# Kernel optimization log

Measured on AMD Instinct MI355X. Metric: run time of the kernel, lower is better.

The kernel has to match this reference:

```python
import jax, jax.numpy as jnp
import numpy as np

B, S, DM, H, NL, DFF = 2, 1024, 1024, 16, 4, 4096
HD = DM // H
MAX_LEN = 1024
NUM_REL = 2 * MAX_LEN - 1
EPS = 1e-5


def setup_inputs() -> dict:
    key = jax.random.key(0)
    ks = jax.random.split(key, 10)
    w = lambda k, shp: jax.random.normal(k, shp, jnp.float32) * 0.02
    return {
        "x": jax.random.normal(ks[0], (B, S, DM), jnp.float32),
        "Wq": w(ks[1], (NL, DM, DM)), "bq": jnp.zeros((NL, DM), jnp.float32),
        "Wk": w(ks[2], (NL, DM, DM)), "bk": jnp.zeros((NL, DM), jnp.float32),
        "Wv": w(ks[3], (NL, DM, DM)), "bv": jnp.zeros((NL, DM), jnp.float32),
        "Wo": w(ks[4], (NL, DM, DM)), "bo": jnp.zeros((NL, DM), jnp.float32),
        "rel": w(ks[5], (NL, NUM_REL, HD)),
        "W1": w(ks[6], (NL, DFF, DM)), "b1": jnp.zeros((NL, DFF), jnp.float32),
        "W2": w(ks[7], (NL, DM, DFF)), "b2": jnp.zeros((NL, DM), jnp.float32),
        "g1": jnp.ones((NL, DM), jnp.float32), "beta1": jnp.zeros((NL, DM), jnp.float32),
        "g2": jnp.ones((NL, DM), jnp.float32), "beta2": jnp.zeros((NL, DM), jnp.float32),
    }


def _layer_norm(y, g, b):
    m = y.mean(-1, keepdims=True)
    v = ((y - m) ** 2).mean(-1, keepdims=True)
    return (y - m) / jnp.sqrt(v + EPS) * g + b


def _forward(x, Wq, bq, Wk, bk, Wv, bv, Wo, bo, rel, W1, b1, W2, b2, g1, beta1, g2, beta2):
    scale = np.sqrt(HD).astype(np.float32)
    # relative position index matrix: idx[j,k] = k - j + S - 1  (values in [0, 2S-2])
    idx = (jnp.arange(S)[None, :] - jnp.arange(S)[:, None]) + S - 1

    def layer(xc, p):
        (Wq_, bq_, Wk_, bk_, Wv_, bv_, Wo_, bo_, rel_,
         W1_, b1_, W2_, b2_, g1_, be1_, g2_, be2_) = p

        def proj(W, b):
            return (xc @ W.T + b).reshape(B, S, H, HD).transpose(0, 2, 1, 3)  # [B,H,S,HD]

        Q, K, V = proj(Wq_, bq_), proj(Wk_, bk_), proj(Wv_, bv_)
        scores = jnp.einsum('bhid,bhjd->bhij', Q, K) / scale
        # einsum('bhid,jkd->bhijk', Q, rel[idx]).mean(-1) == Q @ mean_k(rel[idx])^T
        Ebar = rel_[idx].mean(axis=1)  # [S, HD]
        scores = scores + jnp.einsum('bhid,jd->bhij', Q, Ebar)
        attn = jax.nn.softmax(scores, axis=-1)
        out = jnp.einsum('bhij,bhjd->bhid', attn, V)
        out = out.transpose(0, 2, 1, 3).reshape(B, S, DM) @ Wo_.T + bo_
        xc = _layer_norm(xc + out, g1_, be1_)
        h = jax.nn.gelu(xc @ W1_.T + b1_, approximate=False)
        ff = h @ W2_.T + b2_
        xc = _layer_norm(xc + ff, g2_, be2_)
        return xc, None

    stacked = (Wq, bq, Wk, bk, Wv, bv, Wo, bo, rel, W1, b1, W2, b2, g1, beta1, g2, beta2)
    out, _ = jax.lax.scan(layer, x, stacked)
    return out


def reference(x, Wq, bq, Wk, bk, Wv, bv, Wo, bo, rel, W1, b1, W2, b2, g1, beta1, g2, beta2):
    return _forward(x, Wq, bq, Wk, bk, Wv, bv, Wo, bo, rel, W1, b1, W2, b2, g1, beta1, g2, beta2)
```

## Files before the change

### kernel.cpp

```cpp
#include <hip/hip_runtime.h>
#include <math.h>

typedef __attribute__((ext_vector_type(4))) float f32x4;
typedef __attribute__((ext_vector_type(8))) short s16x8;
typedef __attribute__((ext_vector_type(8))) unsigned short u16x8;
typedef __attribute__((ext_vector_type(4))) unsigned short u16x4;

#define DI __device__ __forceinline__

DI unsigned short f2bf(float f) {
  unsigned int u = __builtin_bit_cast(unsigned int, f);
  u = u + 0x7fffu + ((u >> 16) & 1u);
  return (unsigned short)(u >> 16);
}

DI void gload16(const unsigned short* g, unsigned short* l) {
  __builtin_amdgcn_global_load_lds(
      (const __attribute__((address_space(1))) void*)g,
      (__attribute__((address_space(3))) void*)l, 16, 0, 0);
}

__global__ __launch_bounds__(256) void cvtw_k(const float* __restrict__ src,
    unsigned short* __restrict__ dst, int chunk, int dstStride, int total4)
{
  for (int i = blockIdx.x * 256 + threadIdx.x; i < total4; i += gridDim.x * 256) {
    int idx = i * 4;
    int blk = idx / chunk, off = idx - blk * chunk;
    f32x4 v = *reinterpret_cast<const f32x4*>(src + idx);
    u16x4 o = { f2bf(v[0]), f2bf(v[1]), f2bf(v[2]), f2bf(v[3]) };
    *reinterpret_cast<u16x4*>(dst + (size_t)blk * dstStride + off) = o;
  }
}

__global__ __launch_bounds__(256) void xinit_k(const float* __restrict__ x,
    float* __restrict__ xf, unsigned short* __restrict__ xb, int n4)
{
  for (int i = blockIdx.x * 256 + threadIdx.x; i < n4; i += gridDim.x * 256) {
    f32x4 v = *reinterpret_cast<const f32x4*>(x + (size_t)i * 4);
    *reinterpret_cast<f32x4*>(xf + (size_t)i * 4) = v;
    u16x4 o = { f2bf(v[0]), f2bf(v[1]), f2bf(v[2]), f2bf(v[3]) };
    *reinterpret_cast<u16x4*>(xb + (size_t)i * 4) = o;
  }
}

__global__ __launch_bounds__(64) void ebch_k(const float* __restrict__ rel,
    float* __restrict__ cs)
{
  int c = blockIdx.x, L = blockIdx.y, d = threadIdx.x;
  const float* p = rel + ((size_t)L * 2047 + c * 64) * 64 + d;
  int n = (c == 31) ? 63 : 64;
  float s = 0.f;
  for (int k = 0; k < n; ++k) s += p[(size_t)k * 64];
  cs[(L * 32 + c) * 64 + d] = s;
}

__global__ __launch_bounds__(64) void ebar_k(const float* __restrict__ rel,
    const float* __restrict__ cs, float* __restrict__ ebar4)
{
  int j = blockIdx.x, L = blockIdx.y, d = threadIdx.x;
  int s = 1023 - j, e = s + 1024;
  int c0 = (s + 63) >> 6, c1 = e >> 6;
  const float* rl = rel + (size_t)L * 2047 * 64;
  const float* cl = cs + L * 32 * 64;
  float acc = 0.f;
  for (int c = c0; c < c1; ++c) acc += cl[c * 64 + d];
  for (int t = s; t < c0 * 64; ++t) acc += rl[(size_t)t * 64 + d];
  for (int t = c1 * 64; t < e; ++t) acc += rl[(size_t)t * 64 + d];
  ebar4[((size_t)L * 1024 + j) * 64 + d] = acc * (1.f / 1024.f);
}

template<int BF32, int BN>
__global__ __launch_bounds__(256) void gemm_k(
    const unsigned short* __restrict__ A, const void* __restrict__ Bp,
    int K, int N, int mode, int kLen,
    const float* __restrict__ bias0, const float* __restrict__ bias1,
    const float* __restrict__ bias2, const float* __restrict__ ebar,
    unsigned short* __restrict__ qb, unsigned short* __restrict__ kb,
    unsigned short* __restrict__ vtb, float* __restrict__ yf,
    unsigned short* __restrict__ hb)
{
  constexpr int NI = BN / 32;
  constexpr int WC = BN / 2;
  constexpr int SMSZ = (128 + BN) * 64 > 128 * (BN + 8) ? (128 + BN) * 64 : 128 * (BN + 8);
  __shared__ __align__(16) unsigned short SM[SMSZ];
  auto As = reinterpret_cast<unsigned short(*)[64]>(SM);
  auto Bs = reinterpret_cast<unsigned short(*)[64]>(SM + 128 * 64);
  const int tid = threadIdx.x, l = tid & 63, w = tid >> 6;
  const int wr = w >> 1, wc = w & 1, lr = l & 15, lg = l >> 4;
  const int m0 = blockIdx.y * 128, n0 = blockIdx.x * BN;
  f32x4 acc[4][NI];
#pragma unroll
  for (int i = 0; i < 4; ++i)
#pragma unroll
    for (int j = 0; j < NI; ++j) acc[i][j] = f32x4{0.f, 0.f, 0.f, 0.f};

  const int kBeg = blockIdx.z * kLen, kEnd = kBeg + kLen;
  const unsigned short* gaBase = A + (size_t)(m0 + (l >> 3)) * K + (l & 7) * 8;

  for (int k0 = kBeg; k0 < kEnd; k0 += 64) {
    __syncthreads();
#pragma unroll
    for (int it = 0; it < 4; ++it) {
      int r0 = (w * 4 + it) * 8;
      gload16(gaBase + (size_t)r0 * K + k0, &As[r0][0]);
    }
    if (BF32 == 0) {
      const unsigned short* Bb = (const unsigned short*)Bp;
      const unsigned short* gb = Bb + (size_t)(n0 + (l >> 3)) * K + k0 + (l & 7) * 8;
#pragma unroll
      for (int it = 0; it < BN / 32; ++it) {
        int r0 = (w * (BN / 32) + it) * 8;
        gload16(gb + (size_t)r0 * K, &Bs[r0][0]);
      }
    } else {
      const float* Bf = (const float*)Bp;
#pragma unroll
      for (int it = 0; it < BN / 16; ++it) {
        int lin = (it * 256 + tid) * 4, r = lin >> 6, c = lin & 63;
        f32x4 v = *reinterpret_cast<const f32x4*>(Bf + (size_t)(n0 + r) * K + k0 + c);
        u16x4 o = { f2bf(v[0]), f2bf(v[1]), f2bf(v[2]), f2bf(v[3]) };
        *reinterpret_cast<u16x4*>(&Bs[r][c]) = o;
      }
    }
    __syncthreads();
#pragma unroll
    for (int kk = 0; kk < 2; ++kk) {
      s16x8 af[4], bfr[NI];
#pragma unroll
      for (int mi = 0; mi < 4; ++mi)
        af[mi] = *reinterpret_cast<const s16x8*>(&As[wr * 64 + mi * 16 + lr][kk * 32 + lg * 8]);
#pragma unroll
      for (int ni = 0; ni < NI; ++ni)
        bfr[ni] = *reinterpret_cast<const s16x8*>(&Bs[wc * WC + ni * 16 + lr][kk * 32 + lg * 8]);
#pragma unroll
      for (int mi = 0; mi < 4; ++mi)
#pragma unroll
        for (int ni = 0; ni < NI; ++ni)
          acc[mi][ni] = __builtin_amdgcn_mfma_f32_16x16x32_bf16(af[mi], bfr[ni], acc[mi][ni], 0, 0, 0);
    }
  }

  if (mode <= 3) {
    int qtype, nbase;
    const float* bias;
    if (mode == 0) {
      qtype = n0 >> 10; nbase = n0 & 1023;
      bias = qtype == 0 ? bias0 : (qtype == 1 ? bias1 : bias2);
    } else { qtype = mode - 1; nbase = n0; bias = bias0; }
    if (qtype < 2) {
      unsigned short* dst = (qtype == 0) ? qb : kb;
#pragma unroll
      for (int mi = 0; mi < 4; ++mi)
#pragma unroll
        for (int ni = 0; ni < NI; ++ni) {
          int nin = nbase + wc * WC + ni * 16 + lr;
          int hh = nin >> 6, dh = nin & 63;
          float bv = bias[nin];
#pragma unroll
          for (int rr = 0; rr < 4; ++rr) {
            int m = m0 + wr * 64 + mi * 16 + lg * 4 + rr;
            int b = m >> 10, s = m & 1023;
            float v = acc[mi][ni][rr] + bv;
            if (qtype == 1) v = v * 0.125f + ebar[s * 64 + dh];
            dst[(size_t)(b * 16 + hh) * 65536 + (size_t)s * 64 + dh] = f2bf(v);
          }
        }
    } else {
      auto T = reinterpret_cast<unsigned short(*)[BN + 8]>(SM);
      __syncthreads();
#pragma unroll
      for (int mi = 0; mi < 4; ++mi)
#pragma unroll
        for (int ni = 0; ni < NI; ++ni) {
          int nl = wc * WC + ni * 16 + lr;
          float bv = bias[nbase + nl];
#pragma unroll
          for (int rr = 0; rr < 4; ++rr) {
            int ml = wr * 64 + mi * 16 + lg * 4 + rr;
            T[ml][nl] = f2bf(acc[mi][ni][rr] + bv);
          }
        }
      __syncthreads();
      int b = m0 >> 10, j0 = m0 & 1023;
#pragma unroll
      for (int lp = 0; lp < BN / 16; ++lp) {
        int dl = lp * 16 + (tid >> 4), jc = (tid & 15) * 8;
        u16x8 o;
#pragma unroll
        for (int e = 0; e < 8; ++e) o[e] = T[jc + e][dl];
        int nin = nbase + dl, hh = nin >> 6, dh = nin & 63;
        *reinterpret_cast<u16x8*>(vtb + (size_t)(b * 16 + hh) * 65536 + (size_t)dh * 1024 + j0 + jc) = o;
      }
    }
  } else {
    float* yfp = yf + (size_t)blockIdx.z * 2097152;
#pragma unroll
    for (int mi = 0; mi < 4; ++mi)
#pragma unroll
      for (int ni = 0; ni < NI; ++ni) {
        int nn = n0 + wc * WC + ni * 16 + lr;
        float bv = (blockIdx.z == 0) ? bias0[nn] : 0.f;
#pragma unroll
        for (int rr = 0; rr < 4; ++rr) {
          int m = m0 + wr * 64 + mi * 16 + lg * 4 + rr;
          float v = acc[mi][ni][rr] + bv;
          if (mode == 4) yfp[(size_t)m * N + nn] = v;
          else hb[(size_t)m * N + nn] = f2bf(0.5f * v * (1.f + erff(v * 0.70710678118654752f)));
        }
      }
  }
}

__global__ __launch_bounds__(256, 4) void attn_k(const unsigned short* __restrict__ qb,
    const unsigned short* __restrict__ kb, const unsigned short* __restrict__ vtb,
    float* __restrict__ opart, float* __restrict__ lpart)
{
  __shared__ __align__(16) unsigned short Ks[2][64][72];
  __shared__ __align__(16) unsigned short Vs[64][72];
  __shared__ __align__(16) unsigned short Pl[4][16][72];
  const int id = blockIdx.x;
  const int xcd = id & 7, sub = id >> 3;
  const int bh = xcd * 4 + (sub >> 5);
  const int rest = sub & 31;
  const int tq = rest >> 1, half = rest & 1;
  const int tid = threadIdx.x, l = tid & 63, w = tid >> 6;
  const int lr = l & 15, lg = l >> 4;
  const int jt0 = half * 8;

  const unsigned short* Kb = kb + (size_t)bh * 65536;
  const unsigned short* Vb = vtb + (size_t)bh * 65536;

  const unsigned short* Qp = qb + (size_t)bh * 65536 +
      (size_t)(tq * 64 + w * 16 + lr) * 64 + lg * 8;
  s16x8 qf0 = *reinterpret_cast<const s16x8*>(Qp);
  s16x8 qf1 = *reinterpret_cast<const s16x8*>(Qp + 32);

  const int srow = tid >> 2, scol = (tid & 3) * 16;
  const unsigned short* kg = Kb + (size_t)srow * 64 + scol + (size_t)jt0 * 4096;
  const unsigned short* vg = Vb + (size_t)srow * 1024 + scol + (size_t)jt0 * 64;

  u16x8 krg[2][2], vrg[2][2];
  f32x4 oacc[4];
#pragma unroll
  for (int di = 0; di < 4; ++di) oacc[di] = f32x4{0.f, 0.f, 0.f, 0.f};
  float Lp[4] = { 0.f, 0.f, 0.f, 0.f };

  krg[0][0] = *reinterpret_cast<const u16x8*>(kg);
  krg[0][1] = *reinterpret_cast<const u16x8*>(kg + 8);
  vrg[0][0] = *reinterpret_cast<const u16x8*>(vg);
  vrg[0][1] = *reinterpret_cast<const u16x8*>(vg + 8);
  *reinterpret_cast<u16x8*>(&Ks[0][srow][scol]) = krg[0][0];
  *reinterpret_cast<u16x8*>(&Ks[0][srow][scol + 8]) = krg[0][1];
  krg[1][0] = *reinterpret_cast<const u16x8*>(kg + 4096);
  krg[1][1] = *reinterpret_cast<const u16x8*>(kg + 4096 + 8);
  vrg[1][0] = *reinterpret_cast<const u16x8*>(vg + 64);
  vrg[1][1] = *reinterpret_cast<const u16x8*>(vg + 64 + 8);

#pragma unroll
  for (int it = 0; it < 8; ++it) {
    const int buf = it & 1, nxt = buf ^ 1;
    asm volatile("s_waitcnt lgkmcnt(0)" ::: "memory");
    __builtin_amdgcn_s_barrier();
    __builtin_amdgcn_sched_barrier(0);
    *reinterpret_cast<u16x8*>(&Vs[srow][scol]) = vrg[buf][0];
    *reinterpret_cast<u16x8*>(&Vs[srow][scol + 8]) = vrg[buf][1];
    f32x4 sacc[4];
#pragma unroll
    for (int ni = 0; ni < 4; ++ni) sacc[ni] = f32x4{0.f, 0.f, 0.f, 0.f};
#pragma unroll
    for (int kk = 0; kk < 2; ++kk) {
      s16x8 qq = kk ? qf1 : qf0;
#pragma unroll
      for (int ni = 0; ni < 4; ++ni) {
        s16x8 kf = *reinterpret_cast<const s16x8*>(&Ks[buf][ni * 16 + lr][kk * 32 + lg * 8]);
        sacc[ni] = __builtin_amdgcn_mfma_f32_16x16x32_bf16(qq, kf, sacc[ni], 0, 0, 0);
      }
    }
#pragma unroll
    for (int r = 0; r < 4; ++r) {
#pragma unroll
      for (int ni = 0; ni < 4; ++ni) {
        float p = __expf(fminf(sacc[ni][r], 80.f));
        Lp[r] += p;
        Pl[w][lg * 4 + r][ni * 16 + lr] = f2bf(p);
      }
    }
    asm volatile("s_waitcnt lgkmcnt(0)" ::: "memory");
    __builtin_amdgcn_s_barrier();
    __builtin_amdgcn_sched_barrier(0);
#pragma unroll
    for (int kk = 0; kk < 2; ++kk) {
      s16x8 pa = *reinterpret_cast<const s16x8*>(&Pl[w][lr][kk * 32 + lg * 8]);
#pragma unroll
      for (int di = 0; di < 4; ++di) {
        s16x8 vf = *reinterpret_cast<const s16x8*>(&Vs[di * 16 + lr][kk * 32 + lg * 8]);
        oacc[di] = __builtin_amdgcn_mfma_f32_16x16x32_bf16(pa, vf, oacc[di], 0, 0, 0);
      }
    }
    if (it < 7) {
      *reinterpret_cast<u16x8*>(&Ks[nxt][srow][scol]) = krg[nxt][0];
      *reinterpret_cast<u16x8*>(&Ks[nxt][srow][scol + 8]) = krg[nxt][1];
    }
    if (it < 6) {
      const unsigned short* kp = kg + (size_t)(it + 2) * 4096;
      const unsigned short* vp = vg + (size_t)(it + 2) * 64;
      krg[buf][0] = *reinterpret_cast<const u16x8*>(kp);
      krg[buf][1] = *reinterpret_cast<const u16x8*>(kp + 8);
      vrg[buf][0] = *reinterpret_cast<const u16x8*>(vp);
      vrg[buf][1] = *reinterpret_cast<const u16x8*>(vp + 8);
    }
  }

#pragma unroll
  for (int r = 0; r < 4; ++r) {
#pragma unroll
    for (int xm = 1; xm < 16; xm <<= 1) Lp[r] += __shfl_xor(Lp[r], xm);
  }
  const size_t obase = ((size_t)(half * 32 + bh) * 1024 + tq * 64 + w * 16);
#pragma unroll
  for (int r = 0; r < 4; ++r) {
    int qrow = lg * 4 + r;
#pragma unroll
    for (int di = 0; di < 4; ++di)
      opart[(obase + qrow) * 64 + di * 16 + lr] = oacc[di][r];
    if (lr == 0) lpart[obase + qrow] = Lp[r];
  }
}

__global__ __launch_bounds__(256) void amrg_k(const float* __restrict__ opart,
    const float* __restrict__ lpart, unsigned short* __restrict__ ctx)
{
  int e4 = blockIdx.x * 256 + threadIdx.x;
  int d4 = e4 & 15, q = (e4 >> 4) & 1023, bh = e4 >> 14;
  size_t po = ((size_t)bh * 1024 + q) * 64 + d4 * 4;
  f32x4 o0 = *reinterpret_cast<const f32x4*>(opart + po);
  f32x4 o1 = *reinterpret_cast<const f32x4*>(opart + 2097152 + po);
  float linv = 1.f / (lpart[bh * 1024 + q] + lpart[32768 + bh * 1024 + q]);
  int b = bh >> 4, h = bh & 15;
  u16x4 o;
#pragma unroll
  for (int e = 0; e < 4; ++e) o[e] = f2bf((o0[e] + o1[e]) * linv);
  *reinterpret_cast<u16x4*>(ctx + (size_t)(b * 1024 + q) * 1024 + h * 64 + d4 * 4) = o;
}

__global__ __launch_bounds__(256) void ln_k(const float* __restrict__ xf,
    const float* __restrict__ yf, const float* __restrict__ g,
    const float* __restrict__ be, float* __restrict__ outf,
    unsigned short* __restrict__ outb)
{
  int row = blockIdx.x, tid = threadIdx.x, l = tid & 63, w = tid >> 6;
  size_t base = (size_t)row * 1024 + tid * 4;
  f32x4 v = *reinterpret_cast<const f32x4*>(xf + base);
  f32x4 y0 = *reinterpret_cast<const f32x4*>(yf + base);
  f32x4 y1 = *reinterpret_cast<const f32x4*>(yf + 2097152 + base);
  v = v + y0 + y1;
  float s = v[0] + v[1] + v[2] + v[3];
  float q = v[0] * v[0] + v[1] * v[1] + v[2] * v[2] + v[3] * v[3];
#pragma unroll
  for (int off = 1; off < 64; off <<= 1) { s += __shfl_xor(s, off); q += __shfl_xor(q, off); }
  __shared__ float ss[4], qq[4];
  if (l == 0) { ss[w] = s; qq[w] = q; }
  __syncthreads();
  s = ss[0] + ss[1] + ss[2] + ss[3];
  q = qq[0] + qq[1] + qq[2] + qq[3];
  float m = s * (1.f / 1024.f);
  float var = q * (1.f / 1024.f) - m * m;
  float rs = rsqrtf(var + 1e-5f);
  f32x4 gv = *reinterpret_cast<const f32x4*>(g + tid * 4);
  f32x4 bv = *reinterpret_cast<const f32x4*>(be + tid * 4);
  f32x4 o; u16x4 ob;
#pragma unroll
  for (int e = 0; e < 4; ++e) { o[e] = (v[e] - m) * rs * gv[e] + bv[e]; ob[e] = f2bf(o[e]); }
  *reinterpret_cast<f32x4*>(outf + base) = o;
  *reinterpret_cast<u16x4*>(outb + base) = ob;
}

extern "C" void kernel_launch(void* const* d_in, const int* in_sizes, int n_in,
                              void* d_out, int out_size, void* d_ws, size_t ws_size,
                              hipStream_t stream)
{
  (void)in_sizes; (void)n_in; (void)out_size;
  const float* x   = (const float*)d_in[0];
  const float* Wq  = (const float*)d_in[1];
  const float* bq  = (const float*)d_in[2];
  const float* Wk  = (const float*)d_in[3];
  const float* bk  = (const float*)d_in[4];
  const float* Wv  = (const float*)d_in[5];
  const float* bv  = (const float*)d_in[6];
  const float* Wo  = (const float*)d_in[7];
  const float* bo  = (const float*)d_in[8];
  const float* rel = (const float*)d_in[9];
  const float* W1  = (const float*)d_in[10];
  const float* b1  = (const float*)d_in[11];
  const float* W2  = (const float*)d_in[12];
  const float* b2  = (const float*)d_in[13];
  const float* g1  = (const float*)d_in[14];
  const float* be1 = (const float*)d_in[15];
  const float* g2  = (const float*)d_in[16];
  const float* be2 = (const float*)d_in[17];
  float* out = (float*)d_out;
  char* ws = (char*)d_ws;

  const size_t OFF_XF = 0, OFF_YF = 8388608, OFF_XB = 25165824, OFF_QB = 29360128,
      OFF_KB = 33554432, OFF_VT = 37748736, OFF_CT = 41943040,
      OFF_HB = 46137344 ,
      OFF_LP = 62914560, OFF_EB = 63176704, OFF_CS = 64225280, OFF_W = 64258048;
  const size_t NEED_A = OFF_W + 100663296, NEED_B = OFF_W + 25165824;

  float* xf = (float*)(ws + OFF_XF);
  float* yf = (float*)(ws + OFF_YF);
  unsigned short* xb  = (unsigned short*)(ws + OFF_XB);
  unsigned short* qbp = (unsigned short*)(ws + OFF_QB);
  unsigned short* kbp = (unsigned short*)(ws + OFF_KB);
  unsigned short* vtp = (unsigned short*)(ws + OFF_VT);
  unsigned short* ctx = (unsigned short*)(ws + OFF_CT);
  unsigned short* hb  = (unsigned short*)(ws + OFF_HB);
  float* opart = (float*)(ws + OFF_HB);
  float* lpart = (float*)(ws + OFF_LP);
  float* ebar4 = (float*)(ws + OFF_EB);
  float* csum  = (float*)(ws + OFF_CS);
  unsigned short* wb = (unsigned short*)(ws + OFF_W);

  const int tier = (ws_size >= NEED_A) ? 0 : (ws_size >= NEED_B ? 1 : 2);

  if (tier == 0) {
    cvtw_k<<<2048, 256, 0, stream>>>(Wq, wb,           1048576, 3145728, 1048576);
    cvtw_k<<<2048, 256, 0, stream>>>(Wk, wb + 1048576, 1048576, 3145728, 1048576);
    cvtw_k<<<2048, 256, 0, stream>>>(Wv, wb + 2097152, 1048576, 3145728, 1048576);
    cvtw_k<<<2048, 256, 0, stream>>>(Wo, wb + 12582912, 1048576, 1048576, 1048576);
    cvtw_k<<<2048, 256, 0, stream>>>(W1, wb + 16777216, 4194304, 4194304, 4194304);
    cvtw_k<<<2048, 256, 0, stream>>>(W2, wb + 33554432, 4194304, 4194304, 4194304);
  }
  xinit_k<<<2048, 256, 0, stream>>>(x, xf, xb, 524288);
  ebch_k<<<dim3(32, 4), 64, 0, stream>>>(rel, csum);
  ebar_k<<<dim3(1024, 4), 64, 0, stream>>>(rel, csum, ebar4);

  for (int lyr = 0; lyr < 4; ++lyr) {
    const float* eb = ebar4 + (size_t)lyr * 65536;
    const unsigned short *wqkvP, *woP, *w1P, *w2P;
    if (tier == 0) {
      wqkvP = wb + (size_t)lyr * 3145728;
      woP   = wb + 12582912 + (size_t)lyr * 1048576;
      w1P   = wb + 16777216 + (size_t)lyr * 4194304;
      w2P   = wb + 33554432 + (size_t)lyr * 4194304;
    } else if (tier == 1) {
      wqkvP = wb; woP = wb + 3145728; w1P = wb + 4194304; w2P = wb + 8388608;
      cvtw_k<<<1024, 256, 0, stream>>>(Wq + (size_t)lyr * 1048576, wb,           1 << 30, 0, 262144);
      cvtw_k<<<1024, 256, 0, stream>>>(Wk + (size_t)lyr * 1048576, wb + 1048576, 1 << 30, 0, 262144);
      cvtw_k<<<1024, 256, 0, stream>>>(Wv + (size_t)lyr * 1048576, wb + 2097152, 1 << 30, 0, 262144);
      cvtw_k<<<1024, 256, 0, stream>>>(Wo + (size_t)lyr * 1048576, wb + 3145728, 1 << 30, 0, 262144);
      cvtw_k<<<2048, 256, 0, stream>>>(W1 + (size_t)lyr * 4194304, wb + 4194304, 1 << 30, 0, 1048576);
      cvtw_k<<<2048, 256, 0, stream>>>(W2 + (size_t)lyr * 4194304, wb + 8388608, 1 << 30, 0, 1048576);
    } else { wqkvP = woP = w1P = w2P = nullptr; }

    if (tier <= 1) {
      gemm_k<0, 64><<<dim3(48, 16), 256, 0, stream>>>(xb, wqkvP, 1024, 3072, 0, 1024,
          bq + lyr * 1024, bk + lyr * 1024, bv + lyr * 1024, eb, qbp, kbp, vtp, nullptr, nullptr);
    } else {
      gemm_k<1, 128><<<dim3(8, 16), 256, 0, stream>>>(xb, Wq + (size_t)lyr * 1048576, 1024, 1024, 1, 1024,
          bq + lyr * 1024, nullptr, nullptr, eb, qbp, kbp, vtp, nullptr, nullptr);
      gemm_k<1, 128><<<dim3(8, 16), 256, 0, stream>>>(xb, Wk + (size_t)lyr * 1048576, 1024, 1024, 2, 1024,
          bk + lyr * 1024, nullptr, nullptr, eb, qbp, kbp, vtp, nullptr, nullptr);
      gemm_k<1, 128><<<dim3(8, 16), 256, 0, stream>>>(xb, Wv + (size_t)lyr * 1048576, 1024, 1024, 3, 1024,
          bv + lyr * 1024, nullptr, nullptr, eb, qbp, kbp, vtp, nullptr, nullptr);
    }

    attn_k<<<1024, 256, 0, stream>>>(qbp, kbp, vtp, opart, lpart);
    amrg_k<<<2048, 256, 0, stream>>>(opart, lpart, ctx);

    if (tier <= 1)
      gemm_k<0, 64><<<dim3(16, 16, 2), 256, 0, stream>>>(ctx, woP, 1024, 1024, 4, 512,
          bo + lyr * 1024, nullptr, nullptr, nullptr, nullptr, nullptr, nullptr, yf, nullptr);
    else
      gemm_k<1, 64><<<dim3(16, 16, 2), 256, 0, stream>>>(ctx, Wo + (size_t)lyr * 1048576, 1024, 1024, 4, 512,
          bo + lyr * 1024, nullptr, nullptr, nullptr, nullptr, nullptr, nullptr, yf, nullptr);

    ln_k<<<2048, 256, 0, stream>>>(xf, yf, g1 + lyr * 1024, be1 + lyr * 1024, xf, xb);

    if (tier <= 1)
      gemm_k<0, 128><<<dim3(32, 16), 256, 0, stream>>>(xb, w1P, 1024, 4096, 5, 1024,
          b1 + lyr * 4096, nullptr, nullptr, nullptr, nullptr, nullptr, nullptr, nullptr, hb);
    else
      gemm_k<1, 128><<<dim3(32, 16), 256, 0, stream>>>(xb, W1 + (size_t)lyr * 4194304, 1024, 4096, 5, 1024,
          b1 + lyr * 4096, nullptr, nullptr, nullptr, nullptr, nullptr, nullptr, nullptr, hb);

    if (tier <= 1)
      gemm_k<0, 64><<<dim3(16, 16, 2), 256, 0, stream>>>(hb, w2P, 4096, 1024, 4, 2048,
          b2 + lyr * 1024, nullptr, nullptr, nullptr, nullptr, nullptr, nullptr, yf, nullptr);
    else
      gemm_k<1, 64><<<dim3(16, 16, 2), 256, 0, stream>>>(hb, W2 + (size_t)lyr * 4194304, 4096, 1024, 4, 2048,
          b2 + lyr * 1024, nullptr, nullptr, nullptr, nullptr, nullptr, nullptr, yf, nullptr);

    ln_k<<<2048, 256, 0, stream>>>(xf, yf, g2 + lyr * 1024, be2 + lyr * 1024,
        (lyr == 3) ? out : xf, xb);
  }
}
```

Before: 960.3 us.

## Double-buffer GEMM shared-memory tiles and XOR-swizzle columns to avoid bank conflicts

Turns the bf16 GEMM main loop into a two-stage pipeline: the next K tile is loaded into a second LDS buffer while MFMAs run on the current one, which removes one barrier per iteration. It also XOR-swizzles the 8-element column chunks by row, on both the global-to-LDS writes and the fragment reads, to cut LDS bank conflicts. LDS use doubles, which may lower occupancy. The epilogue reuses the same shared array and relies on the trailing barrier.

```diff
diff --git a/kernel.cpp b/kernel.cpp
--- a/kernel.cpp
+++ b/kernel.cpp
@@ -81,10 +81,10 @@
 {
   constexpr int NI = BN / 32;
   constexpr int WC = BN / 2;
-  constexpr int SMSZ = (128 + BN) * 64 > 128 * (BN + 8) ? (128 + BN) * 64 : 128 * (BN + 8);
+  constexpr int SMSZ = 2 * (128 + BN) * 64 > 128 * (BN + 8) ? 2 * (128 + BN) * 64 : 128 * (BN + 8);
   __shared__ __align__(16) unsigned short SM[SMSZ];
   auto As = reinterpret_cast<unsigned short(*)[64]>(SM);
-  auto Bs = reinterpret_cast<unsigned short(*)[64]>(SM + 128 * 64);
+  auto Bs = reinterpret_cast<unsigned short(*)[64]>(SM + 2 * 128 * 64);
   const int tid = threadIdx.x, l = tid & 63, w = tid >> 6;
   const int wr = w >> 1, wc = w & 1, lr = l & 15, lg = l >> 4;
   const int m0 = blockIdx.y * 128, n0 = blockIdx.x * BN;
@@ -95,22 +95,23 @@
     for (int j = 0; j < NI; ++j) acc[i][j] = f32x4{0.f, 0.f, 0.f, 0.f};
 
   const int kBeg = blockIdx.z * kLen, kEnd = kBeg + kLen;
-  const unsigned short* gaBase = A + (size_t)(m0 + (l >> 3)) * K + (l & 7) * 8;
-
-  for (int k0 = kBeg; k0 < kEnd; k0 += 64) {
-    __syncthreads();
+  const unsigned short* gaBase = A + (size_t)(m0 + (l >> 3)) * K + ((l & 7) ^ (l >> 3)) * 8;
+  const unsigned short* gbBase = (BF32 == 0)
+      ? (const unsigned short*)Bp + (size_t)(n0 + (l >> 3)) * K + ((l & 7) ^ (l >> 3)) * 8
+      : nullptr;
+  const int csw = (lr & 7) * 8;
+
+  auto STAGE = [&](int cb, int k0) {
 #pragma unroll
     for (int it = 0; it < 4; ++it) {
       int r0 = (w * 4 + it) * 8;
-      gload16(gaBase + (size_t)r0 * K + k0, &As[r0][0]);
-    }
-    if (BF32 == 0) {
-      const unsigned short* Bb = (const unsigned short*)Bp;
-      const unsigned short* gb = Bb + (size_t)(n0 + (l >> 3)) * K + k0 + (l & 7) * 8;
+      gload16(gaBase + (size_t)r0 * K + k0, &As[cb * 128 + r0][0]);
+    }
+    if constexpr (BF32 == 0) {
 #pragma unroll
       for (int it = 0; it < BN / 32; ++it) {
         int r0 = (w * (BN / 32) + it) * 8;
-        gload16(gb + (size_t)r0 * K, &Bs[r0][0]);
+        gload16(gbBase + (size_t)r0 * K + k0, &Bs[cb * BN + r0][0]);
       }
     } else {
       const float* Bf = (const float*)Bp;
@@ -119,25 +120,35 @@
         int lin = (it * 256 + tid) * 4, r = lin >> 6, c = lin & 63;
         f32x4 v = *reinterpret_cast<const f32x4*>(Bf + (size_t)(n0 + r) * K + k0 + c);
         u16x4 o = { f2bf(v[0]), f2bf(v[1]), f2bf(v[2]), f2bf(v[3]) };
-        *reinterpret_cast<u16x4*>(&Bs[r][c]) = o;
-      }
-    }
-    __syncthreads();
+        *reinterpret_cast<u16x4*>(&Bs[cb * BN + r][c ^ ((r & 7) << 3)]) = o;
+      }
+    }
+  };
+
+  STAGE(0, kBeg);
+  __syncthreads();
+  int cur = 0;
+  for (int k0 = kBeg; k0 < kEnd; k0 += 64) {
+    if (k0 + 64 < kEnd) STAGE(cur ^ 1, k0 + 64);
 #pragma unroll
     for (int kk = 0; kk < 2; ++kk) {
       s16x8 af[4], bfr[NI];
 #pragma unroll
       for (int mi = 0; mi < 4; ++mi)
-        af[mi] = *reinterpret_cast<const s16x8*>(&As[wr * 64 + mi * 16 + lr][kk * 32 + lg * 8]);
+        af[mi] = *reinterpret_cast<const s16x8*>(
+            &As[cur * 128 + wr * 64 + mi * 16 + lr][(kk * 32 + lg * 8) ^ csw]);
 #pragma unroll
       for (int ni = 0; ni < NI; ++ni)
-        bfr[ni] = *reinterpret_cast<const s16x8*>(&Bs[wc * WC + ni * 16 + lr][kk * 32 + lg * 8]);
+        bfr[ni] = *reinterpret_cast<const s16x8*>(
+            &Bs[cur * BN + wc * WC + ni * 16 + lr][(kk * 32 + lg * 8) ^ csw]);
 #pragma unroll
       for (int mi = 0; mi < 4; ++mi)
 #pragma unroll
         for (int ni = 0; ni < NI; ++ni)
           acc[mi][ni] = __builtin_amdgcn_mfma_f32_16x16x32_bf16(af[mi], bfr[ni], acc[mi][ni], 0, 0, 0);
     }
+    __syncthreads();
+    cur ^= 1;
   }
 
   if (mode <= 3) {
@@ -403,8 +414,8 @@
 
   const size_t OFF_XF = 0, OFF_YF = 8388608, OFF_XB = 25165824, OFF_QB = 29360128,
       OFF_KB = 33554432, OFF_VT = 37748736, OFF_CT = 41943040,
-      OFF_HB = 46137344 ,
-      OFF_LP = 62914560, OFF_EB = 63176704, OFF_CS = 64225280, OFF_W = 64258048;
+      OFF_HB = 46137344, OFF_LP = 62914560, OFF_EB = 63176704,
+      OFF_CS = 64225280, OFF_W = 64258048;
   const size_t NEED_A = OFF_W + 100663296, NEED_B = OFF_W + 25165824;
 
   float* xf = (float*)(ws + OFF_XF);
```

New measurement: 834.9 us. 1.15x faster.
